# Optimization experiments

Hardware: AMD Instinct MI355X
Metric: run time of the kernel (lower is better)

Reference implementation:

```python
import jax, jax.numpy as jnp
import numpy as np

BATCH, SEQ, INPUT_SIZE, RESERVOIR = 32, 2048, 256, 512


def setup_inputs() -> dict:
    key = jax.random.key(0)
    k_x, k_w, k_d = jax.random.split(key, 3)
    x = jax.random.normal(k_x, (BATCH, SEQ, INPUT_SIZE), dtype=jnp.float32)
    # input_projection weight: uniform(-1, 1), shape [R, input_size]
    W_in = jax.random.uniform(k_w, (RESERVOIR, INPUT_SIZE), dtype=jnp.float32, minval=-1.0, maxval=1.0)
    # diagonal of state_projection: uniform(-0.5, 0.5)
    d = jax.random.uniform(k_d, (RESERVOIR,), dtype=jnp.float32, minval=-0.5, maxval=0.5)
    return {"x": x, "W_in": W_in, "d": d}


def reference(x, W_in, d):
    B, T, _ = x.shape
    R = d.shape[0]
    # input projection: [B, T, R]
    u = jnp.einsum('bti,ri->btr', x, W_in)

    # recurrence: state_t = tanh(d * state_{t-1} + u_t)  (leak gate is dead code: 0*old + 1*new)
    # torch loop fills indices 1..T-1 of all_states (T+1 slots), then returns [:, 1:],
    # so the final returned timestep is all zeros.
    def step(state, u_t):
        new_state = jnp.tanh(d * state + u_t)
        return new_state, new_state

    init = jnp.zeros((B, R), dtype=x.dtype)
    u_tm = jnp.swapaxes(u[:, 1:, :], 0, 1)  # time-major [T-1, B, R]
    _, states = jax.lax.scan(step, init, u_tm)
    states = jnp.swapaxes(states, 0, 1)  # [B, T-1, R]
    tail = jnp.zeros((B, 1, R), dtype=x.dtype)
    return jnp.concatenate([states, tail], axis=1)  # [B, T, R]
```

## Files before the change

### kernel.cpp

```cpp
#include <hip/hip_runtime.h>

#define BATCH 32
#define SEQT  2048
#define INSZ  256
#define RSV   512
#define MTOT  (BATCH * SEQT)
#define BM 128
#define BN 128
#define BK 32
#define LSA 40
#define LSB 72

using f16x8 = __attribute__((ext_vector_type(8))) _Float16;
using f16x4 = __attribute__((ext_vector_type(4))) _Float16;
using f32x4 = __attribute__((ext_vector_type(4))) float;

__global__ __launch_bounds__(256) void esn_gemm(const float* __restrict__ X,
                                                const float* __restrict__ W,
                                                float* __restrict__ U) {
    __shared__ _Float16 Ash[BM * LSA];
    __shared__ _Float16 Bsh[BN * LSB];

    const int tid  = threadIdx.x;
    const int lane = tid & 63;
    const int wid  = tid >> 6;
    const int wr   = wid >> 1, wc = wid & 1;
    const int bm   = blockIdx.x >> 2, bn = blockIdx.x & 3;

    const int srow = tid >> 3;
    const int scol = (tid & 7) * 4;

    f32x4 acc[4][4] = {};

    for (int ks = 0; ks < INSZ / BK; ++ks) {
        __syncthreads();
        #pragma unroll
        for (int p = 0; p < 4; ++p) {
            const int row = srow + p * 32;
            float4 av = *(const float4*)(X + (size_t)(bm * BM + row) * INSZ + ks * BK + scol);
            float4 bv = *(const float4*)(W + (size_t)(bn * BN + row) * INSZ + ks * BK + scol);
            float a4[4] = {av.x, av.y, av.z, av.w};
            float b4[4] = {bv.x, bv.y, bv.z, bv.w};
            f16x4 ah, bh, bl;
            #pragma unroll
            for (int j = 0; j < 4; ++j) {
                ah[j] = (_Float16)a4[j];
                _Float16 h = (_Float16)b4[j];
                bh[j] = h;
                bl[j] = (_Float16)(b4[j] - (float)h);
            }
            *(f16x4*)&Ash[row * LSA + scol] = ah;
            *(f16x4*)&Bsh[row * LSB + scol] = bh;
            *(f16x4*)&Bsh[row * LSB + 32 + scol] = bl;
        }
        __syncthreads();

        f16x8 af[4], bfh[4], bfl[4];
        #pragma unroll
        for (int m = 0; m < 4; ++m)
            af[m] = *(const f16x8*)&Ash[(wr * 64 + m * 16 + (lane & 15)) * LSA + (lane >> 4) * 8];
        #pragma unroll
        for (int n = 0; n < 4; ++n) {
            const _Float16* p = &Bsh[(wc * 64 + n * 16 + (lane & 15)) * LSB + (lane >> 4) * 8];
            bfh[n] = *(const f16x8*)p;
            bfl[n] = *(const f16x8*)(p + 32);
        }
        #pragma unroll
        for (int m = 0; m < 4; ++m)
            #pragma unroll
            for (int n = 0; n < 4; ++n) {
                acc[m][n] = __builtin_amdgcn_mfma_f32_16x16x32_f16(af[m], bfh[n], acc[m][n], 0, 0, 0);
                acc[m][n] = __builtin_amdgcn_mfma_f32_16x16x32_f16(af[m], bfl[n], acc[m][n], 0, 0, 0);
            }
    }

    #pragma unroll
    for (int m = 0; m < 4; ++m) {
        const int row = bm * BM + wr * 64 + m * 16 + (lane >> 4) * 4;
        #pragma unroll
        for (int n = 0; n < 4; ++n) {
            const int col = bn * BN + wc * 64 + n * 16 + (lane & 15);
            f32x4 v = acc[m][n];
            #pragma unroll
            for (int j = 0; j < 4; ++j)
                U[(size_t)(row + j) * RSV + col] = v[j];
        }
    }
}

#define K2LOG2E 2.8853900817779268f

#define STEP(uv, tt) do {                                   \
    float z  = __builtin_fmaf(dK, s, (uv) * K2LOG2E);       \
    float p  = __builtin_amdgcn_exp2f(z);                   \
    float rc = __builtin_amdgcn_rcpf(1.0f + p);             \
    s = __builtin_fmaf(-2.0f, rc, 1.0f);                    \
    base[(size_t)(tt) * RSV] = s;                           \
} while (0)

#define PROC8(buf, t0) do {                                 \
    _Pragma("unroll")                                       \
    for (int j = 0; j < 8; ++j) {                           \
        STEP(buf[j], (t0) + j);                             \
        int idx = (t0) + 33 + j;                            \
        idx = idx < SEQT ? idx : SEQT - 1;                  \
        buf[j] = base[(size_t)idx * RSV];                   \
    }                                                       \
} while (0)

__global__ __launch_bounds__(64) void esn_recur(float* __restrict__ OUT,
                                                const float* __restrict__ D) {
    const int gid = blockIdx.x * 64 + threadIdx.x;
    const int b = gid >> 9;
    const int r = gid & (RSV - 1);
    float* base = OUT + (size_t)b * SEQT * RSV + r;
    const float dK = D[r] * K2LOG2E;
    float s = 0.0f;

    float bA[8], bB[8], bC[8], bD[8];
    #pragma unroll
    for (int j = 0; j < 8; ++j) bA[j] = base[(size_t)(1 + j) * RSV];
    #pragma unroll
    for (int j = 0; j < 8; ++j) bB[j] = base[(size_t)(9 + j) * RSV];
    #pragma unroll
    for (int j = 0; j < 8; ++j) bC[j] = base[(size_t)(17 + j) * RSV];
    #pragma unroll
    for (int j = 0; j < 8; ++j) bD[j] = base[(size_t)(25 + j) * RSV];

    int t = 0;
    for (int it = 0; it < 63; ++it) {
        PROC8(bA, t);
        PROC8(bB, t + 8);
        PROC8(bC, t + 16);
        PROC8(bD, t + 24);
        t += 32;
    }
    #pragma unroll
    for (int j = 0; j < 8; ++j) STEP(bA[j], 2016 + j);
    #pragma unroll
    for (int j = 0; j < 8; ++j) STEP(bB[j], 2024 + j);
    #pragma unroll
    for (int j = 0; j < 8; ++j) STEP(bC[j], 2032 + j);
    #pragma unroll
    for (int j = 0; j < 7; ++j) STEP(bD[j], 2040 + j);

    base[(size_t)(SEQT - 1) * RSV] = 0.0f;
}

extern "C" void kernel_launch(void* const* d_in, const int* in_sizes, int n_in,
                              void* d_out, int out_size, void* d_ws, size_t ws_size,
                              hipStream_t stream) {
    const float* X = (const float*)d_in[0];
    const float* W = (const float*)d_in[1];
    const float* D = (const float*)d_in[2];
    float* OUT = (float*)d_out;

    esn_gemm<<<dim3((MTOT / BM) * (RSV / BN)), dim3(256), 0, stream>>>(X, W, OUT);
    esn_recur<<<dim3(BATCH * RSV / 64), dim3(64), 0, stream>>>(OUT, D);
}
```

Measured before the change: 278.8 us.

## Split recurrence into warm-started time segments with fp16 transposed U workspace

Adds a pre-pass that converts W into split fp16 hi/lo halves once, loaded into LDS with global_load_lds. The GEMM now writes U as fp16 in a transposed, time-contiguous workspace with a remapped block order. The recurrence is split into 8 time segments per batch. Each segment warm-starts from zero over 32 prior steps, relying on the contraction of tanh with |d|<0.5, which exposes more parallelism and shortens the serial chain. The approximations (fp16 U and truncated warm-up) risk accuracy, and the extra kernel launch adds a small cost.

After: 299.1 us. 7.3% more time.

```diff
diff --git a/kernel.cpp b/kernel.cpp
--- a/kernel.cpp
+++ b/kernel.cpp
@@ -9,24 +9,177 @@
 #define BN 128
 #define BK 32
 #define LSA 40
-#define LSB 72
+#define PADM 65600
+
+#define K2LOG2E 2.8853900817779268f
 
 using f16x8 = __attribute__((ext_vector_type(8))) _Float16;
 using f16x4 = __attribute__((ext_vector_type(4))) _Float16;
 using f32x4 = __attribute__((ext_vector_type(4))) float;
 
-__global__ __launch_bounds__(256) void esn_gemm(const float* __restrict__ X,
-                                                const float* __restrict__ W,
-                                                float* __restrict__ U) {
+typedef __attribute__((address_space(1))) unsigned int as1_u32;
+typedef __attribute__((address_space(3))) unsigned int as3_u32;
+#define GLDS16(gp, lp) __builtin_amdgcn_global_load_lds((as1_u32*)(gp), (as3_u32*)(lp), 16, 0, 0)
+
+static __device__ __forceinline__ float esn_step(float s, float u, float dK) {
+    float z  = __builtin_fmaf(dK, s, u * K2LOG2E);
+    float e  = __builtin_amdgcn_exp2f(z);
+    float rc = __builtin_amdgcn_rcpf(1.0f + e);
+    return __builtin_fmaf(-2.0f, rc, 1.0f);
+}
+
+
+__global__ __launch_bounds__(256) void esn_convw(const float* __restrict__ W,
+                                                 _Float16* __restrict__ W16) {
+    const int i = blockIdx.x * 256 + threadIdx.x;
+    float4 v = *(const float4*)(W + (size_t)i * 4);
+    float w4[4] = {v.x, v.y, v.z, v.w};
+    f16x4 h, l;
+    #pragma unroll
+    for (int j = 0; j < 4; ++j) {
+        _Float16 hh = (_Float16)w4[j];
+        h[j] = hh;
+        l[j] = (_Float16)(w4[j] - (float)hh);
+    }
+    *(f16x4*)(W16 + (size_t)i * 4) = h;
+    *(f16x4*)(W16 + (size_t)RSV * INSZ + (size_t)i * 4) = l;
+}
+
+__global__ __launch_bounds__(256) void esn_gemm_f(const float* __restrict__ X,
+                                                  const _Float16* __restrict__ W16,
+                                                  _Float16* __restrict__ U16T) {
     __shared__ _Float16 Ash[BM * LSA];
-    __shared__ _Float16 Bsh[BN * LSB];
+    __shared__ _Float16 Bh[BM * BK];
+    __shared__ _Float16 Bl[BM * BK];
+
+    const int tid  = threadIdx.x;
+    const int lane = tid & 63;
+    const int wid  = tid >> 6;
+    const int wr   = wid >> 1, wc = wid & 1;
+    const int lgc = (blockIdx.x & 7) * 256 + (blockIdx.x >> 3);
+    const int bm = lgc >> 2, bn = lgc & 3;
+
+    const int srow = tid >> 3;
+    const int scol = (tid & 7) * 4;
+
+    f32x4 acc[4][4] = {};
+
+    for (int ks = 0; ks < INSZ / BK; ++ks) {
+        __syncthreads();
+        #pragma unroll
+        for (int q = 0; q < 2; ++q) {
+            const int c   = (wid * 2 + q) * 64 + lane;
+            const int row = c >> 2, col = (c & 3) * 8;
+            const _Float16* gh = W16 + (size_t)(bn * BM + row) * INSZ + ks * BK + col;
+            GLDS16(gh, &Bh[(wid * 2 + q) * 512]);
+            GLDS16(gh + (size_t)RSV * INSZ, &Bl[(wid * 2 + q) * 512]);
+        }
+        #pragma unroll
+        for (int p = 0; p < 4; ++p) {
+            const int row = srow + p * 32;
+            float4 av = *(const float4*)(X + (size_t)(bm * BM + row) * INSZ + ks * BK + scol);
+            float a4[4] = {av.x, av.y, av.z, av.w};
+            f16x4 ah;
+            #pragma unroll
+            for (int j = 0; j < 4; ++j) ah[j] = (_Float16)a4[j];
+            *(f16x4*)&Ash[row * LSA + scol] = ah;
+        }
+        __syncthreads();
+
+        f16x8 af[4], bfh[4], bfl[4];
+        #pragma unroll
+        for (int m = 0; m < 4; ++m)
+            af[m] = *(const f16x8*)&Ash[(wr * 64 + m * 16 + (lane & 15)) * LSA + (lane >> 4) * 8];
+        #pragma unroll
+        for (int n = 0; n < 4; ++n) {
+            const int rr = (wc * 64 + n * 16 + (lane & 15)) * BK + (lane >> 4) * 8;
+            bfh[n] = *(const f16x8*)&Bh[rr];
+            bfl[n] = *(const f16x8*)&Bl[rr];
+        }
+        #pragma unroll
+        for (int m = 0; m < 4; ++m)
+            #pragma unroll
+            for (int n = 0; n < 4; ++n) {
+                acc[m][n] = __builtin_amdgcn_mfma_f32_16x16x32_f16(af[m], bfh[n], acc[m][n], 0, 0, 0);
+                acc[m][n] = __builtin_amdgcn_mfma_f32_16x16x32_f16(af[m], bfl[n], acc[m][n], 0, 0, 0);
+            }
+    }
+
+    #pragma unroll
+    for (int m = 0; m < 4; ++m) {
+        const int row0 = bm * BM + wr * 64 + m * 16 + (lane >> 4) * 4;
+        #pragma unroll
+        for (int n = 0; n < 4; ++n) {
+            const int col = bn * BN + wc * 64 + n * 16 + (lane & 15);
+            f32x4 v = acc[m][n];
+            f16x4 o;
+            #pragma unroll
+            for (int j = 0; j < 4; ++j) o[j] = (_Float16)v[j];
+            *(f16x4*)(U16T + (size_t)col * PADM + row0) = o;
+        }
+    }
+}
+
+__global__ __launch_bounds__(256) void esn_recur_f(const _Float16* __restrict__ U16T,
+                                                   const float* __restrict__ D,
+                                                   float* __restrict__ OUT) {
+    const int tid  = threadIdx.x;
+    const int half = blockIdx.x & 1;
+    const int pair = blockIdx.x >> 1;
+    const int b    = pair >> 3, seg = pair & 7;
+    const int r    = half * 256 + tid;
+
+    const _Float16* urow = U16T + (size_t)r * PADM + b * SEQT;
+    float* obase = OUT + (size_t)b * SEQT * RSV + r;
+    const float dK = D[r] * K2LOG2E;
+    const int t0 = seg * 256;
+
+    float s = 0.0f;
+    if (seg) {
+        #pragma unroll
+        for (int k = 0; k < 32; ++k)
+            s = esn_step(s, (float)urow[t0 - 31 + k], dK);
+    }
+
+    _Float16 bufA[8], bufB[8];
+    #pragma unroll
+    for (int j = 0; j < 8; ++j) bufA[j] = urow[t0 + 1 + j];
+    #pragma unroll
+    for (int j = 0; j < 8; ++j) bufB[j] = urow[t0 + 9 + j];
+
+#define PROC8F(buf, tt) do {                                  \
+    _Pragma("unroll")                                         \
+    for (int j = 0; j < 8; ++j) {                             \
+        s = esn_step(s, (float)buf[j], dK);                   \
+        obase[(size_t)((tt) + j) * RSV] = s;                  \
+        int idx = (tt) + j + 17;                              \
+        idx = idx < SEQT ? idx : SEQT - 1;                    \
+        buf[j] = urow[idx];                                   \
+    }                                                         \
+} while (0)
+
+    int t = t0;
+    for (int it = 0; it < 16; ++it) {
+        PROC8F(bufA, t);
+        PROC8F(bufB, t + 8);
+        t += 16;
+    }
+#undef PROC8F
+    if (seg == 7) obase[(size_t)(SEQT - 1) * RSV] = 0.0f;
+}
+
+
+__global__ __launch_bounds__(256) void esn_gemm_fb(const float* __restrict__ X,
+                                                   const float* __restrict__ W,
+                                                   float* __restrict__ U) {
+    __shared__ _Float16 Ash[BM * LSA];
+    __shared__ _Float16 Bsh[BN * 72];
 
     const int tid  = threadIdx.x;
     const int lane = tid & 63;
     const int wid  = tid >> 6;
     const int wr   = wid >> 1, wc = wid & 1;
     const int bm   = blockIdx.x >> 2, bn = blockIdx.x & 3;
-
     const int srow = tid >> 3;
     const int scol = (tid & 7) * 4;
 
@@ -50,8 +203,8 @@
                 bl[j] = (_Float16)(b4[j] - (float)h);
             }
             *(f16x4*)&Ash[row * LSA + scol] = ah;
-            *(f16x4*)&Bsh[row * LSB + scol] = bh;
-            *(f16x4*)&Bsh[row * LSB + 32 + scol] = bl;
+            *(f16x4*)&Bsh[row * 72 + scol] = bh;
+            *(f16x4*)&Bsh[row * 72 + 32 + scol] = bl;
         }
         __syncthreads();
 
@@ -61,7 +214,7 @@
             af[m] = *(const f16x8*)&Ash[(wr * 64 + m * 16 + (lane & 15)) * LSA + (lane >> 4) * 8];
         #pragma unroll
         for (int n = 0; n < 4; ++n) {
-            const _Float16* p = &Bsh[(wc * 64 + n * 16 + (lane & 15)) * LSB + (lane >> 4) * 8];
+            const _Float16* p = &Bsh[(wc * 64 + n * 16 + (lane & 15)) * 72 + (lane >> 4) * 8];
             bfh[n] = *(const f16x8*)p;
             bfl[n] = *(const f16x8*)(p + 32);
         }
@@ -88,28 +241,8 @@
     }
 }
 
-#define K2LOG2E 2.8853900817779268f
-
-#define STEP(uv, tt) do {                                   \
-    float z  = __builtin_fmaf(dK, s, (uv) * K2LOG2E);       \
-    float p  = __builtin_amdgcn_exp2f(z);                   \
-    float rc = __builtin_amdgcn_rcpf(1.0f + p);             \
-    s = __builtin_fmaf(-2.0f, rc, 1.0f);                    \
-    base[(size_t)(tt) * RSV] = s;                           \
-} while (0)
-
-#define PROC8(buf, t0) do {                                 \
-    _Pragma("unroll")                                       \
-    for (int j = 0; j < 8; ++j) {                           \
-        STEP(buf[j], (t0) + j);                             \
-        int idx = (t0) + 33 + j;                            \
-        idx = idx < SEQT ? idx : SEQT - 1;                  \
-        buf[j] = base[(size_t)idx * RSV];                   \
-    }                                                       \
-} while (0)
-
-__global__ __launch_bounds__(64) void esn_recur(float* __restrict__ OUT,
-                                                const float* __restrict__ D) {
+__global__ __launch_bounds__(64) void esn_recur_fb(float* __restrict__ OUT,
+                                                   const float* __restrict__ D) {
     const int gid = blockIdx.x * 64 + threadIdx.x;
     const int b = gid >> 9;
     const int r = gid & (RSV - 1);
@@ -127,22 +260,34 @@
     #pragma unroll
     for (int j = 0; j < 8; ++j) bD[j] = base[(size_t)(25 + j) * RSV];
 
+#define PROC8B(buf, tt) do {                                  \
+    _Pragma("unroll")                                         \
+    for (int j = 0; j < 8; ++j) {                             \
+        s = esn_step(s, buf[j], dK);                          \
+        base[(size_t)((tt) + j) * RSV] = s;                   \
+        int idx = (tt) + 33 + j;                              \
+        idx = idx < SEQT ? idx : SEQT - 1;                    \
+        buf[j] = base[(size_t)idx * RSV];                     \
+    }                                                         \
+} while (0)
+
     int t = 0;
     for (int it = 0; it < 63; ++it) {
-        PROC8(bA, t);
-        PROC8(bB, t + 8);
-        PROC8(bC, t + 16);
-        PROC8(bD, t + 24);
+        PROC8B(bA, t);
+        PROC8B(bB, t + 8);
+        PROC8B(bC, t + 16);
+        PROC8B(bD, t + 24);
         t += 32;
     }
-    #pragma unroll
-    for (int j = 0; j < 8; ++j) STEP(bA[j], 2016 + j);
-    #pragma unroll
-    for (int j = 0; j < 8; ++j) STEP(bB[j], 2024 + j);
-    #pragma unroll
-    for (int j = 0; j < 8; ++j) STEP(bC[j], 2032 + j);
-    #pragma unroll
-    for (int j = 0; j < 7; ++j) STEP(bD[j], 2040 + j);
+#undef PROC8B
+    #pragma unroll
+    for (int j = 0; j < 8; ++j) { s = esn_step(s, bA[j], dK); base[(size_t)(2016 + j) * RSV] = s; }
+    #pragma unroll
+    for (int j = 0; j < 8; ++j) { s = esn_step(s, bB[j], dK); base[(size_t)(2024 + j) * RSV] = s; }
+    #pragma unroll
+    for (int j = 0; j < 8; ++j) { s = esn_step(s, bC[j], dK); base[(size_t)(2032 + j) * RSV] = s; }
+    #pragma unroll
+    for (int j = 0; j < 7; ++j) { s = esn_step(s, bD[j], dK); base[(size_t)(2040 + j) * RSV] = s; }
 
     base[(size_t)(SEQT - 1) * RSV] = 0.0f;
 }
@@ -155,6 +300,16 @@
     const float* D = (const float*)d_in[2];
     float* OUT = (float*)d_out;
 
-    esn_gemm<<<dim3((MTOT / BM) * (RSV / BN)), dim3(256), 0, stream>>>(X, W, OUT);
-    esn_recur<<<dim3(BATCH * RSV / 64), dim3(64), 0, stream>>>(OUT, D);
-}
+    const size_t W16_BYTES  = (size_t)2 * RSV * INSZ * sizeof(_Float16);
+    const size_t U16T_BYTES = (size_t)RSV * PADM * sizeof(_Float16);
+    if (ws_size >= W16_BYTES + U16T_BYTES) {
+        _Float16* W16  = (_Float16*)d_ws;
+        _Float16* U16T = (_Float16*)((char*)d_ws + W16_BYTES);
+        esn_convw<<<dim3(RSV * INSZ / 4 / 256), dim3(256), 0, stream>>>(W, W16);
+        esn_gemm_f<<<dim3((MTOT / BM) * (RSV / BN)), dim3(256), 0, stream>>>(X, W16, U16T);
+        esn_recur_f<<<dim3(BATCH * 8 * 2), dim3(256), 0, stream>>>(U16T, D, OUT);
+    } else {
+        esn_gemm_fb<<<dim3((MTOT / BM) * (RSV / BN)), dim3(256), 0, stream>>>(X, W, OUT);
+        esn_recur_fb<<<dim3(BATCH * RSV / 64), dim3(64), 0, stream>>>(OUT, D);
+    }
+}
```
